# Performance work log

Hardware: AMD Instinct MI355X
Metric: run time of the kernel (lower is better)

## Reference

```python
import jax, jax.numpy as jnp
import numpy as np

FEAT = 3136          # conved_channel//8 * pooled_size**2 = 512//8 * 7*7
HIDDEN = 64
NUM_CLASSES = 21
SELECTED_PROPOSAL = 128
LEAKY_SLOPE = 0.1


def leaky_relu(x, slope=LEAKY_SLOPE):
    return jnp.where(x >= 0, x, slope * x)


def setup_inputs() -> dict:
    key = jax.random.key(0)
    k_x, k_kc, k_w1, k_b1, k_w2, k_b2 = jax.random.split(key, 6)
    B, R = 64, 300
    x = jax.random.normal(k_x, (B, R, FEAT), dtype=jnp.float32)
    keep_count = jax.random.randint(k_kc, (B,), 0, R, dtype=jnp.int32)
    # nn.Linear default init: U(-1/sqrt(fan_in), 1/sqrt(fan_in))
    bnd1 = 1.0 / np.sqrt(FEAT)
    W1 = jax.random.uniform(k_w1, (FEAT, HIDDEN), jnp.float32, -bnd1, bnd1)
    b1 = jax.random.uniform(k_b1, (HIDDEN,), jnp.float32, -bnd1, bnd1)
    bnd2 = 1.0 / np.sqrt(HIDDEN)
    W2 = jax.random.uniform(k_w2, (HIDDEN, NUM_CLASSES), jnp.float32, -bnd2, bnd2)
    b2 = jax.random.uniform(k_b2, (NUM_CLASSES,), jnp.float32, -bnd2, bnd2)
    return {"x": x, "W1": W1, "b1": b1, "W2": W2, "b2": b2, "keep_count": keep_count}


def reference(x, W1, b1, W2, b2, keep_count):
    # x: [B, R, FEAT]; only the first SELECTED_PROPOSAL ROIs can be written.
    B = x.shape[0]
    S = SELECTED_PROPOSAL
    xs = x.reshape(B, x.shape[1], -1)[:, :S, :]                 # [B, S, F]
    h = leaky_relu(jnp.einsum('bsf,fh->bsh', xs, W1) + b1)      # [B, S, 64]
    # Dropout(0.25) is identity in eval mode.
    out = leaky_relu(jnp.einsum('bsh,hk->bsk', h, W2) + b2)     # [B, S, K]
    # rows j >= min(keep_count[idx], S) stay zero
    limit = jnp.minimum(keep_count, S)                          # [B]
    mask = jnp.arange(S)[None, :] < limit[:, None]              # [B, S]
    return jnp.where(mask[:, :, None], out, jnp.zeros((), out.dtype))
```

## Files before the change

### kernel.cpp

```cpp
#include <hip/hip_runtime.h>
#include <hip/hip_bf16.h>

static constexpr int FEAT_  = 3136;
static constexpr int KSTEPS = 98;
static constexpr int RSTR   = 300;
static constexpr int SROWS  = 128;
static constexpr int HID    = 64;
static constexpr int NCLS   = 21;
static constexpr int BM     = 32;

typedef __attribute__((ext_vector_type(8))) short bf16x8;
typedef __attribute__((ext_vector_type(4))) float f32x4;

__device__ bf16x8 g_w1p[KSTEPS * 4 * 64];

__device__ __forceinline__ short f2bf(float f) {
    union { float f; unsigned u; } v; v.f = f;
    unsigned r = v.u + 0x7fffu + ((v.u >> 16) & 1u);
    return (short)(r >> 16);
}

__global__ __launch_bounds__(256) void pack_w1(const float* __restrict__ W1) {
    int t = blockIdx.x * 256 + threadIdx.x;
    int lane = t & 63;
    int nt   = (t >> 6) & 3;
    int ks   = t >> 8;
    int col  = nt * 16 + (lane & 15);
    int g    = lane >> 4;
    int k0   = ks * 32 + g * 4;
    bf16x8 v;
    #pragma unroll
    for (int j = 0; j < 4; ++j) v[j]     = f2bf(W1[(k0 + j) * HID + col]);
    #pragma unroll
    for (int j = 0; j < 4; ++j) v[4 + j] = f2bf(W1[(k0 + 16 + j) * HID + col]);
    g_w1p[t] = v;
}

__global__ __launch_bounds__(512) void fused_main(
    const float* __restrict__ x,  const float* __restrict__ b1,
    const float* __restrict__ W2, const float* __restrict__ b2,
    const int*  __restrict__ keep, float* __restrict__ out)
{
    const int tid  = threadIdx.x;
    const int lane = tid & 63;
    const int wv   = tid >> 6;
    const int row_base = blockIdx.x * BM;
    const int b      = row_base >> 7;
    const int s_base = row_base & 127;

    float* outp = out + row_base * NCLS;
    const int limit = min(keep[b], SROWS);

    if (s_base >= limit) {
        for (int i = tid; i < BM * NCLS; i += 512) outp[i] = 0.f;
        return;
    }

    __shared__ float hp[8][BM][HID + 1];
    __shared__ float hf[BM][HID + 2];
    __shared__ float w2s[HID * NCLS];

    for (int i = tid; i < HID * NCLS; i += 512) w2s[i] = W2[i];

    const int ks0 = (wv * KSTEPS) >> 3;
    const int ks1 = ((wv + 1) * KSTEPS) >> 3;

    const int g = lane >> 4;
    const int r = lane & 15;
    const int row0 = min(s_base + r,      limit - 1);
    const int row1 = min(s_base + 16 + r, limit - 1);
    const float* xp0 = x + (b * RSTR + row0) * FEAT_ + g * 4;
    const float* xp1 = x + (b * RSTR + row1) * FEAT_ + g * 4;
    const bf16x8* wp = g_w1p + lane;

    f32x4 a00 = {0,0,0,0}, a01 = {0,0,0,0}, a02 = {0,0,0,0}, a03 = {0,0,0,0};
    f32x4 a10 = {0,0,0,0}, a11 = {0,0,0,0}, a12 = {0,0,0,0}, a13 = {0,0,0,0};

    #pragma unroll 2
    for (int ks = ks0; ks < ks1; ++ks) {
        float4 p0a = *(const float4*)(xp0 + ks * 32);
        float4 p0b = *(const float4*)(xp0 + ks * 32 + 16);
        float4 p1a = *(const float4*)(xp1 + ks * 32);
        float4 p1b = *(const float4*)(xp1 + ks * 32 + 16);
        bf16x8 bv0 = wp[(ks * 4 + 0) * 64];
        bf16x8 bv1 = wp[(ks * 4 + 1) * 64];
        bf16x8 bv2 = wp[(ks * 4 + 2) * 64];
        bf16x8 bv3 = wp[(ks * 4 + 3) * 64];
        bf16x8 af0, af1;
        af0[0]=f2bf(p0a.x); af0[1]=f2bf(p0a.y); af0[2]=f2bf(p0a.z); af0[3]=f2bf(p0a.w);
        af0[4]=f2bf(p0b.x); af0[5]=f2bf(p0b.y); af0[6]=f2bf(p0b.z); af0[7]=f2bf(p0b.w);
        af1[0]=f2bf(p1a.x); af1[1]=f2bf(p1a.y); af1[2]=f2bf(p1a.z); af1[3]=f2bf(p1a.w);
        af1[4]=f2bf(p1b.x); af1[5]=f2bf(p1b.y); af1[6]=f2bf(p1b.z); af1[7]=f2bf(p1b.w);
        a00 = __builtin_amdgcn_mfma_f32_16x16x32_bf16(af0, bv0, a00, 0, 0, 0);
        a01 = __builtin_amdgcn_mfma_f32_16x16x32_bf16(af0, bv1, a01, 0, 0, 0);
        a02 = __builtin_amdgcn_mfma_f32_16x16x32_bf16(af0, bv2, a02, 0, 0, 0);
        a03 = __builtin_amdgcn_mfma_f32_16x16x32_bf16(af0, bv3, a03, 0, 0, 0);
        a10 = __builtin_amdgcn_mfma_f32_16x16x32_bf16(af1, bv0, a10, 0, 0, 0);
        a11 = __builtin_amdgcn_mfma_f32_16x16x32_bf16(af1, bv1, a11, 0, 0, 0);
        a12 = __builtin_amdgcn_mfma_f32_16x16x32_bf16(af1, bv2, a12, 0, 0, 0);
        a13 = __builtin_amdgcn_mfma_f32_16x16x32_bf16(af1, bv3, a13, 0, 0, 0);
    }

    #pragma unroll
    for (int rr = 0; rr < 4; ++rr) {
        const int mr0 = g * 4 + rr, mr1 = 16 + g * 4 + rr;
        hp[wv][mr0][r     ] = a00[rr];
        hp[wv][mr0][r + 16] = a01[rr];
        hp[wv][mr0][r + 32] = a02[rr];
        hp[wv][mr0][r + 48] = a03[rr];
        hp[wv][mr1][r     ] = a10[rr];
        hp[wv][mr1][r + 16] = a11[rr];
        hp[wv][mr1][r + 32] = a12[rr];
        hp[wv][mr1][r + 48] = a13[rr];
    }
    __syncthreads();

    for (int e = tid; e < BM * HID; e += 512) {
        int row = e >> 6, col = e & 63;
        float v = b1[col];
        #pragma unroll
        for (int p = 0; p < 8; ++p) v += hp[p][row][col];
        hf[row][col] = (v >= 0.f) ? v : 0.1f * v;
    }
    __syncthreads();

    for (int idx = tid; idx < BM * NCLS; idx += 512) {
        int rI = idx / NCLS;
        int c  = idx - rI * NCLS;
        float a2 = b2[c];
        #pragma unroll 8
        for (int col = 0; col < HID; ++col)
            a2 += hf[rI][col] * w2s[col * NCLS + c];
        a2 = (a2 >= 0.f) ? a2 : 0.1f * a2;
        outp[idx] = (s_base + rI < limit) ? a2 : 0.f;
    }
}

extern "C" void kernel_launch(void* const* d_in, const int* in_sizes, int n_in,
                              void* d_out, int out_size, void* d_ws, size_t ws_size,
                              hipStream_t stream) {
    const float* x    = (const float*)d_in[0];
    const float* W1   = (const float*)d_in[1];
    const float* b1   = (const float*)d_in[2];
    const float* W2   = (const float*)d_in[3];
    const float* b2   = (const float*)d_in[4];
    const int*   keep = (const int*)d_in[5];
    float* out = (float*)d_out;

    hipLaunchKernelGGL(pack_w1,    dim3(KSTEPS), dim3(256), 0, stream, W1);
    hipLaunchKernelGGL(fused_main, dim3((64 * SROWS) / BM), dim3(512), 0, stream,
                       x, b1, W2, b2, keep, out);
}
```

Measured before the change: 29.03 us.

## Use hardware bf16 pack conversion, nontemporal loads/stores, and deeper K-loop unroll

Replaces the manual integer round-to-nearest bf16 conversion with HIP's paired float2-to-bfloat162 intrinsics, which on MI355X can map to a packed convert instruction and cut VALU work per MFMA input. Streaming x loads and output stores become nontemporal to avoid polluting cache. The main K loop unroll goes from 2 to 4 to expose more loads in flight. Deeper unroll raises register pressure, and nontemporal hints may have little effect since x is read only once.

```diff
diff --git a/kernel.cpp b/kernel.cpp
--- a/kernel.cpp
+++ b/kernel.cpp
@@ -14,12 +14,6 @@
 
 __device__ bf16x8 g_w1p[KSTEPS * 4 * 64];
 
-__device__ __forceinline__ short f2bf(float f) {
-    union { float f; unsigned u; } v; v.f = f;
-    unsigned r = v.u + 0x7fffu + ((v.u >> 16) & 1u);
-    return (short)(r >> 16);
-}
-
 __global__ __launch_bounds__(256) void pack_w1(const float* __restrict__ W1) {
     int t = blockIdx.x * 256 + threadIdx.x;
     int lane = t & 63;
@@ -28,12 +22,28 @@
     int col  = nt * 16 + (lane & 15);
     int g    = lane >> 4;
     int k0   = ks * 32 + g * 4;
-    bf16x8 v;
+    union { bf16x8 v; __hip_bfloat16 h[8]; } u;
     #pragma unroll
-    for (int j = 0; j < 4; ++j) v[j]     = f2bf(W1[(k0 + j) * HID + col]);
+    for (int j = 0; j < 4; ++j)
+        u.h[j] = __float2bfloat16(W1[(k0 + j) * HID + col]);
     #pragma unroll
-    for (int j = 0; j < 4; ++j) v[4 + j] = f2bf(W1[(k0 + 16 + j) * HID + col]);
-    g_w1p[t] = v;
+    for (int j = 0; j < 4; ++j)
+        u.h[4 + j] = __float2bfloat16(W1[(k0 + 16 + j) * HID + col]);
+    g_w1p[t] = u.v;
+}
+
+__device__ __forceinline__ bf16x8 pack8(f32x4 a, f32x4 b) {
+    union { bf16x8 v; __hip_bfloat162 h[4]; } u;
+    u.h[0] = __float22bfloat162_rn(make_float2(a[0], a[1]));
+    u.h[1] = __float22bfloat162_rn(make_float2(a[2], a[3]));
+    u.h[2] = __float22bfloat162_rn(make_float2(b[0], b[1]));
+    u.h[3] = __float22bfloat162_rn(make_float2(b[2], b[3]));
+    return u.v;
+}
+
+__device__ __forceinline__ f32x4 ntld4(const float* p) {
+    const f32x4* q = (const f32x4*)p;
+    return __builtin_nontemporal_load(q);
 }
 
 __global__ __launch_bounds__(512) void fused_main(
@@ -52,7 +62,8 @@
     const int limit = min(keep[b], SROWS);
 
     if (s_base >= limit) {
-        for (int i = tid; i < BM * NCLS; i += 512) outp[i] = 0.f;
+        for (int i = tid; i < BM * NCLS; i += 512)
+            __builtin_nontemporal_store(0.f, &outp[i]);
         return;
     }
 
@@ -76,21 +87,18 @@
     f32x4 a00 = {0,0,0,0}, a01 = {0,0,0,0}, a02 = {0,0,0,0}, a03 = {0,0,0,0};
     f32x4 a10 = {0,0,0,0}, a11 = {0,0,0,0}, a12 = {0,0,0,0}, a13 = {0,0,0,0};
 
-    #pragma unroll 2
+    #pragma unroll 4
     for (int ks = ks0; ks < ks1; ++ks) {
-        float4 p0a = *(const float4*)(xp0 + ks * 32);
-        float4 p0b = *(const float4*)(xp0 + ks * 32 + 16);
-        float4 p1a = *(const float4*)(xp1 + ks * 32);
-        float4 p1b = *(const float4*)(xp1 + ks * 32 + 16);
+        f32x4 p0a = ntld4(xp0 + ks * 32);
+        f32x4 p0b = ntld4(xp0 + ks * 32 + 16);
+        f32x4 p1a = ntld4(xp1 + ks * 32);
+        f32x4 p1b = ntld4(xp1 + ks * 32 + 16);
         bf16x8 bv0 = wp[(ks * 4 + 0) * 64];
         bf16x8 bv1 = wp[(ks * 4 + 1) * 64];
         bf16x8 bv2 = wp[(ks * 4 + 2) * 64];
         bf16x8 bv3 = wp[(ks * 4 + 3) * 64];
-        bf16x8 af0, af1;
-        af0[0]=f2bf(p0a.x); af0[1]=f2bf(p0a.y); af0[2]=f2bf(p0a.z); af0[3]=f2bf(p0a.w);
-        af0[4]=f2bf(p0b.x); af0[5]=f2bf(p0b.y); af0[6]=f2bf(p0b.z); af0[7]=f2bf(p0b.w);
-        af1[0]=f2bf(p1a.x); af1[1]=f2bf(p1a.y); af1[2]=f2bf(p1a.z); af1[3]=f2bf(p1a.w);
-        af1[4]=f2bf(p1b.x); af1[5]=f2bf(p1b.y); af1[6]=f2bf(p1b.z); af1[7]=f2bf(p1b.w);
+        bf16x8 af0 = pack8(p0a, p0b);
+        bf16x8 af1 = pack8(p1a, p1b);
         a00 = __builtin_amdgcn_mfma_f32_16x16x32_bf16(af0, bv0, a00, 0, 0, 0);
         a01 = __builtin_amdgcn_mfma_f32_16x16x32_bf16(af0, bv1, a01, 0, 0, 0);
         a02 = __builtin_amdgcn_mfma_f32_16x16x32_bf16(af0, bv2, a02, 0, 0, 0);
@@ -132,7 +140,8 @@
         for (int col = 0; col < HID; ++col)
             a2 += hf[rI][col] * w2s[col * NCLS + c];
         a2 = (a2 >= 0.f) ? a2 : 0.1f * a2;
-        outp[idx] = (s_base + rI < limit) ? a2 : 0.f;
+        float res = (s_base + rI < limit) ? a2 : 0.f;
+        __builtin_nontemporal_store(res, &outp[idx]);
     }
 }
 
```

After: 38.16 us. +31.5%, slower.
